# Kernel optimization log

Measured on AMD Instinct MI355X. Metric: run time of the kernel, lower is better.

The kernel has to match this reference:

```python
import jax, jax.numpy as jnp
import numpy as np
from jax import lax

B, N, CIN, COUT, FPS, K, TCH, M, H = 8, 4096, 128, 256, 1024, 24, 256, 32, 4
HD = TCH // H
BN_SCALE = 1.0 / np.sqrt(1.0 + 1e-5)  # eval-mode BN: running_mean=0, running_var=1


def _gather(points, idx):
    # points [B,N,C], idx [B,S] or [B,S,K] -> gathered points
    return jax.vmap(lambda p, i: p[i])(points, idx)


def _bn(x, g, b):
    return x * (g * BN_SCALE) + b


def _ln(x, g, b):
    mu = jnp.mean(x, -1, keepdims=True)
    v = jnp.var(x, -1, keepdims=True)
    return (x - mu) / jnp.sqrt(v + 1e-5) * g + b


def _gelu(x):
    return jax.nn.gelu(x, approximate=False)


def _fps(xyz, npoint, farthest0):
    Bb, Nn, _ = xyz.shape
    def step(carry, _):
        dmin, far = carry
        c = jax.vmap(lambda p, i: p[i])(xyz, far)  # [B,3]
        d = jnp.sum((xyz - c[:, None, :]) ** 2, -1)
        dmin = jnp.minimum(dmin, d)
        return (dmin, jnp.argmax(dmin, -1)), far
    init = (jnp.full((Bb, Nn), 1e10, xyz.dtype), farthest0)
    _, cents = lax.scan(step, init, None, length=npoint)
    return cents.T  # [B, npoint]


def _sqdist(src, dst):
    d = -2.0 * jnp.einsum('bnc,bmc->bnm', src, dst)
    d = d + jnp.sum(src ** 2, -1)[:, :, None]
    d = d + jnp.sum(dst ** 2, -1)[:, None, :]
    return d


def _forward(xyz, x, t, farthest0, Wproj, gproj, bproj, Wl1, gl1, bl1, Wl2, gl2, bl2,
             Wc1, gc1, bc1, Wc2, gc2, bc2, Wq, Wk, Wv, Wo,
             ln1g, ln1b, Wqkv, Wao, ln2g, ln2b, Wf1, Wf2):
    # --- GenerateGraph: FPS + KNN grouping ---
    fps_idx = _fps(xyz, FPS, farthest0)            # [B,S]
    new_xyz = _gather(xyz, fps_idx)                # [B,S,3]
    xT = jnp.transpose(x, (0, 2, 1))               # [B,N,Cin]
    new_pts = _gather(xT, fps_idx)                 # [B,S,Cin]
    dist = _sqdist(new_xyz, xyz)                   # [B,S,N]
    _, idx = lax.top_k(-dist, K)                   # [B,S,K] nearest neighbors
    grouped = _gather(xT, idx)                     # [B,S,K,Cin]
    edge = grouped - new_pts[:, :, None, :]
    # --- Local: Conv1DBR proj + Conv1DBRRes (channels-last, 1x1 convs = GEMM) ---
    h = _gelu(_bn(jnp.einsum('bskc,oc->bsko', edge, Wproj), gproj, bproj))
    r = _gelu(_bn(jnp.einsum('bsko,po->bskp', h, Wl1), gl1, bl1))
    r = _bn(jnp.einsum('bskp,op->bsko', r, Wl2), gl2, bl2)
    h = _gelu(r + h)
    f = jnp.max(h, axis=2)                         # adaptive_max_pool over k -> [B,S,O]
    # --- Channel (ca): Conv1DBRRes on centroid features ---
    r = _gelu(_bn(f @ Wc1.T, gc1, bc1))
    r = _bn(r @ Wc2.T, gc2, bc2)
    f = _gelu(r + f)
    x_out = jnp.transpose(f, (0, 2, 1))            # [B,O,S]
    # --- Local2Former: tokens attend to local features ---
    q = t @ Wq.T
    kk = f @ Wk.T
    v = f @ Wv.T
    a = jax.nn.softmax(jnp.einsum('bmd,bsd->bms', q, kk) * (TCH ** -0.5), axis=-1)
    t = t + jnp.einsum('bms,bsd->bmd', a, v) @ Wo.T
    # --- Former: one pre-norm encoder layer (MHA + MLP) ---
    hn = _ln(t, ln1g, ln1b)
    qkv = (hn @ Wqkv.T).reshape(B, M, 3, H, HD).transpose(2, 0, 3, 1, 4)
    qh, kh, vh = qkv[0], qkv[1], qkv[2]            # [B,H,M,hd]
    attn = jax.nn.softmax(jnp.einsum('bhmd,bhnd->bhmn', qh, kh) * (HD ** -0.5), axis=-1)
    o = jnp.einsum('bhmn,bhnd->bhmd', attn, vh).transpose(0, 2, 1, 3).reshape(B, M, TCH)
    t = t + o @ Wao.T
    hn = _ln(t, ln2g, ln2b)
    t = t + _gelu(hn @ Wf1.T) @ Wf2.T
    return new_xyz, x_out, t


def setup_inputs() -> dict:
    key = jax.random.key(0)
    ks = jax.random.split(key, 40)
    def w(k, o, i):
        return jax.random.normal(k, (o, i), jnp.float32) / np.sqrt(i)
    def g(k, c):
        return 1.0 + 0.1 * jax.random.normal(k, (c,), jnp.float32)
    def bta(k, c):
        return 0.1 * jax.random.normal(k, (c,), jnp.float32)
    inp = {
        'xyz': jax.random.normal(ks[0], (B, N, 3), jnp.float32),
        'x': jax.random.normal(ks[1], (B, CIN, N), jnp.float32),
        't': jax.random.normal(ks[2], (B, M, TCH), jnp.float32),
        'farthest0': jax.random.randint(ks[3], (B,), 0, N),
        'Wproj': w(ks[4], COUT, CIN), 'gproj': g(ks[5], COUT), 'bproj': bta(ks[6], COUT),
        'Wl1': w(ks[7], COUT, COUT), 'gl1': g(ks[8], COUT), 'bl1': bta(ks[9], COUT),
        'Wl2': w(ks[10], COUT, COUT), 'gl2': g(ks[11], COUT), 'bl2': bta(ks[12], COUT),
        'Wc1': w(ks[13], COUT, COUT), 'gc1': g(ks[14], COUT), 'bc1': bta(ks[15], COUT),
        'Wc2': w(ks[16], COUT, COUT), 'gc2': g(ks[17], COUT), 'bc2': bta(ks[18], COUT),
        'Wq': w(ks[19], TCH, TCH), 'Wk': w(ks[20], TCH, COUT), 'Wv': w(ks[21], TCH, COUT),
        'Wo': w(ks[22], TCH, TCH),
        'ln1g': g(ks[23], TCH), 'ln1b': bta(ks[24], TCH),
        'Wqkv': w(ks[25], 3 * TCH, TCH), 'Wao': w(ks[26], TCH, TCH),
        'ln2g': g(ks[27], TCH), 'ln2b': bta(ks[28], TCH),
        'Wf1': w(ks[29], 2 * TCH, TCH), 'Wf2': w(ks[30], TCH, 2 * TCH),
    }
    return inp


def reference(xyz, x, t, farthest0, Wproj, gproj, bproj, Wl1, gl1, bl1, Wl2, gl2, bl2,
              Wc1, gc1, bc1, Wc2, gc2, bc2, Wq, Wk, Wv, Wo,
              ln1g, ln1b, Wqkv, Wao, ln2g, ln2b, Wf1, Wf2):
    return _forward(xyz, x, t, farthest0, Wproj, gproj, bproj, Wl1, gl1, bl1, Wl2, gl2, bl2,
                    Wc1, gc1, bc1, Wc2, gc2, bc2, Wq, Wk, Wv, Wo,
                    ln1g, ln1b, Wqkv, Wao, ln2g, ln2b, Wf1, Wf2)
```

## Files before the change

### kernel.cpp

```cpp
#include <hip/hip_runtime.h>
#include <math.h>

#define Bc 8
#define Nc 4096
#define CINc 128
#define COUTc 256
#define Sc 1024
#define Kc 24
#define TCHc 256
#define Mc 32
#define Hc 4
#define HDc 64
#define MBAT (Sc*Kc)

#define BN_SCALE_F 0.9999950000374997f

typedef __attribute__((ext_vector_type(8))) short bf16x8;
typedef __attribute__((ext_vector_type(4))) float f32x4;

__device__ __forceinline__ float b2f(short s){
  unsigned int u = ((unsigned int)(unsigned short)s) << 16;
  union { unsigned int u; float f; } c; c.u = u; return c.f;
}
__device__ __forceinline__ short f2b(float f){
  union { unsigned int u; float f; } c; c.f = f;
  unsigned int u = c.u;
  unsigned int r = (u + 0x7fffu + ((u >> 16) & 1u)) >> 16;
  return (short)(r & 0xffffu);
}
__device__ __forceinline__ float gelu_f(float v){
  return 0.5f * v * (1.f + erff(v * 0.7071067811865475f));
}
__device__ __forceinline__ float rdval(const float* p){ return *p; }
__device__ __forceinline__ float rdval(const short* p){ return b2f(*p); }
__device__ __forceinline__ void wrval(float* p, float v){ *p = v; }
__device__ __forceinline__ void wrval(short* p, float v){ *p = f2b(v); }

__device__ __forceinline__ void gl_lds16(const short* g, short* l){
  __builtin_amdgcn_global_load_lds(
     (const __attribute__((address_space(1))) void*)g,
     (__attribute__((address_space(3))) void*)l, 16, 0, 0);
}

__device__ __forceinline__ void bar_lds(){
  asm volatile("s_waitcnt lgkmcnt(0)" ::: "memory");
  __builtin_amdgcn_s_barrier();
}

template<int CTRL>
__device__ __forceinline__ double dpp_max_f64(double v){
  long long x = __double_as_longlong(v);
  int lo = (int)(unsigned int)(x & 0xFFFFFFFFLL);
  int hi = (int)(unsigned int)((unsigned long long)x >> 32);
  int plo = __builtin_amdgcn_update_dpp(lo, lo, CTRL, 0xF, 0xF, false);
  int phi = __builtin_amdgcn_update_dpp(hi, hi, CTRL, 0xF, 0xF, false);
  double p = __longlong_as_double((long long)(((unsigned long long)(unsigned int)phi << 32)
                                              | (unsigned int)plo));
  return fmax(v, p);
}
template<int CTRL>
__device__ __forceinline__ float dpp_min_f32(float v){
  int x = __float_as_int(v);
  int p = __builtin_amdgcn_update_dpp(x, x, CTRL, 0xF, 0xF, false);
  return fminf(v, __int_as_float(p));
}
template<int CTRL>
__device__ __forceinline__ float dpp_max_f32(float v){
  int x = __float_as_int(v);
  int p = __builtin_amdgcn_update_dpp(x, x, CTRL, 0xF, 0xF, false);
  return fmaxf(v, __int_as_float(p));
}
template<int CTRL>
__device__ __forceinline__ unsigned dpp_min_u32(unsigned v){
  int p = __builtin_amdgcn_update_dpp((int)v, (int)v, CTRL, 0xF, 0xF, false);
  unsigned pu = (unsigned)p;
  return v < pu ? v : pu;
}
__device__ __forceinline__ float wave_min63(float v){
  v = dpp_min_f32<0x111>(v); v = dpp_min_f32<0x112>(v); v = dpp_min_f32<0x114>(v);
  v = dpp_min_f32<0x118>(v); v = dpp_min_f32<0x142>(v); v = dpp_min_f32<0x143>(v);
  return v;
}
__device__ __forceinline__ float wave_max63(float v){
  v = dpp_max_f32<0x111>(v); v = dpp_max_f32<0x112>(v); v = dpp_max_f32<0x114>(v);
  v = dpp_max_f32<0x118>(v); v = dpp_max_f32<0x142>(v); v = dpp_max_f32<0x143>(v);
  return v;
}
__device__ __forceinline__ float bcast63(float v){
  return __int_as_float(__builtin_amdgcn_readlane(__float_as_int(v), 63));
}

#define PREP_FPS 8
#define PREP_TOTAL 256
#define NWORK 248

__global__ __launch_bounds__(512) void prep_kernel(
    const float* __restrict__ xyz, const int* __restrict__ far0, int* __restrict__ fps_idx,
    const float* __restrict__ x, short* __restrict__ xT,
    const float* __restrict__ Wproj, const float* __restrict__ Wl1, const float* __restrict__ Wl2,
    const float* __restrict__ Wc1, const float* __restrict__ Wc2,
    const float* __restrict__ Wk, const float* __restrict__ Wv,
    const float* __restrict__ Wq, const float* __restrict__ Wo,
    const float* __restrict__ Wqkv, const float* __restrict__ Wao,
    const float* __restrict__ Wf1, const float* __restrict__ Wf2,
    const float* __restrict__ t_in,
    short* __restrict__ wbf,
    int* __restrict__ knn_idx, float* __restrict__ out0){
  __shared__ __align__(16) char smemc[57728];
  int bid = blockIdx.x, tid = threadIdx.x;
  if(bid < PREP_FPS){
    int b = bid;
    float* sxyz = (float*)smemc;
    unsigned short* sid = (unsigned short*)(smemc + 49152);
    int* hist = (int*)(smemc + 57344);
    double* pwave = (double*)(smemc + 57600);
    const float* xb = xyz + (size_t)b*Nc*3;
    if(tid < 64) hist[tid] = 0;
    float gx[8], gy[8], gz[8]; int code[8];
    __syncthreads();
#pragma unroll
    for(int j=0;j<8;j++){
      int n = tid + 512*j;
      const float* p = xb + n*3;
      gx[j]=p[0]; gy[j]=p[1]; gz[j]=p[2];
      int qx = (int)fminf(fmaxf((gx[j]+4.2f)*(4.f/8.4f),0.f),3.f);
      int qy = (int)fminf(fmaxf((gy[j]+4.2f)*(4.f/8.4f),0.f),3.f);
      int qz = (int)fminf(fmaxf((gz[j]+4.2f)*(4.f/8.4f),0.f),3.f);
      code[j] = ((qx>>1)<<5)|((qy>>1)<<4)|((qz>>1)<<3)|((qx&1)<<2)|((qy&1)<<1)|(qz&1);
      atomicAdd(&hist[code[j]], 1);
    }
    __syncthreads();
    if(tid==0){
      int run=0;
      for(int i=0;i<64;i++){ int h=hist[i]; hist[i]=run; run+=h; }
    }
    __syncthreads();
#pragma unroll
    for(int j=0;j<8;j++){
      int slot = atomicAdd(&hist[code[j]], 1);
      sxyz[slot*3]=gx[j]; sxyz[slot*3+1]=gy[j]; sxyz[slot*3+2]=gz[j];
      sid[slot] = (unsigned short)(tid + 512*j);
    }
    __syncthreads();
    float px[8], py[8], pz[8], dmin[8];
    unsigned int lokey[8];
    float mnx=3e38f,mny=3e38f,mnz=3e38f,mxx=-3e38f,mxy=-3e38f,mxz=-3e38f;
#pragma unroll
    for(int j=0;j<8;j++){
      int i = (tid>>6)*512 + j*64 + (tid&63);
      float xx=sxyz[i*3], yy=sxyz[i*3+1], zz=sxyz[i*3+2];
      px[j]=xx; py[j]=yy; pz[j]=zz;
      dmin[j]=1e10f;
      lokey[j]=(unsigned int)((Nc-1) - (int)sid[i]);
      mnx=fminf(mnx,xx); mxx=fmaxf(mxx,xx);
      mny=fminf(mny,yy); mxy=fmaxf(mxy,yy);
      mnz=fminf(mnz,zz); mxz=fmaxf(mxz,zz);
    }
    float bbmnx = bcast63(wave_min63(mnx)), bbmxx = bcast63(wave_max63(mxx));
    float bbmny = bcast63(wave_min63(mny)), bbmxy = bcast63(wave_max63(mxy));
    float bbmnz = bcast63(wave_min63(mnz)), bbmxz = bcast63(wave_max63(mxz));
    __syncthreads();
    for(int i=tid; i<Nc; i+=512){
      const float* p = xb + i*3;
      sxyz[i*3]=p[0]; sxyz[i*3+1]=p[1]; sxyz[i*3+2]=p[2];
    }
    __syncthreads();
    int winner = far0[b] & (Nc-1);
    int* out = fps_idx + b*Sc;
    double pk = 0.0;
    float wm = 3.0e38f;
    for(int it=0; it<Sc; it++){
      if(tid==0)
        __hip_atomic_store(&out[it], winner, __ATOMIC_RELAXED, __HIP_MEMORY_SCOPE_AGENT);
      float cx=sxyz[winner*3], cy=sxyz[winner*3+1], cz=sxyz[winner*3+2];
      float ddx = fmaxf(fmaxf(bbmnx - cx, cx - bbmxx), 0.f);
      float ddy = fmaxf(fmaxf(bbmny - cy, cy - bbmxy), 0.f);
      float ddz = fmaxf(fmaxf(bbmnz - cz, cz - bbmxz), 0.f);
      float md2 = ddx*ddx + ddy*ddy + ddz*ddz;
      if(md2 < wm*1.0001f){
        double key[8];
#pragma unroll
        for(int j=0;j<8;j++){
          float dx = __fsub_rn(px[j], cx);
          float dy = __fsub_rn(py[j], cy);
          float dz = __fsub_rn(pz[j], cz);
          float d = __fadd_rn(__fadd_rn(__fmul_rn(dx,dx), __fmul_rn(dy,dy)), __fmul_rn(dz,dz));
          dmin[j] = fminf(dmin[j], d);
          unsigned long long k = (((unsigned long long)__float_as_uint(dmin[j])) << 32) | lokey[j];
          key[j] = __longlong_as_double((long long)k);
        }
#pragma unroll
        for(int st=4; st>0; st>>=1)
#pragma unroll
          for(int j=0;j<st;j++) key[j] = fmax(key[j], key[j+st]);
        double kv = key[0];
        kv = dpp_max_f64<0x111>(kv);
        kv = dpp_max_f64<0x112>(kv);
        kv = dpp_max_f64<0x114>(kv);
        kv = dpp_max_f64<0x118>(kv);
        kv = dpp_max_f64<0x142>(kv);
        kv = dpp_max_f64<0x143>(kv);
        pk = kv;
        wm = __int_as_float(__builtin_amdgcn_readlane(
               (int)(__double_as_longlong(kv) >> 32), 63));
      }
      int p = it & 1;
      if((tid & 63) == 63) pwave[p*8 + (tid>>6)] = pk;
      bar_lds();
      double k0 = pwave[p*8+0], k1 = pwave[p*8+1], k2 = pwave[p*8+2], k3 = pwave[p*8+3];
      double k4 = pwave[p*8+4], k5 = pwave[p*8+5], k6 = pwave[p*8+6], k7 = pwave[p*8+7];
      double kb = fmax(fmax(fmax(k0,k1), fmax(k2,k3)), fmax(fmax(k4,k5), fmax(k6,k7)));
      unsigned long long kbits = (unsigned long long)__double_as_longlong(kb);
      winner = (Nc-1) - (int)(kbits & 0xFFFFFFFFULL);
    }
  } else {
    int wid = bid - PREP_FPS;
    int b = wid / 31;
    int widb = wid % 31;
    short (*tile)[33] = (short(*)[33])smemc;
    for(int t = wid; t < 4096; t += NWORK){
      int bb = t >> 9;
      int rem = t & 511;
      int n0 = (rem & 127) * 32;
      int c0 = (rem >> 7) * 32;
      int tx = tid & 31, ty = tid >> 5;
      __syncthreads();
#pragma unroll
      for(int i=0;i<32;i+=16)
        tile[ty+i][tx] = f2b(x[((size_t)bb*CINc + (c0+ty+i))*Nc + n0+tx]);
      __syncthreads();
#pragma unroll
      for(int i=0;i<32;i+=16)
        xT[((size_t)bb*Nc + (n0+ty+i))*CINc + c0+tx] = tile[tx][ty+i];
    }
    {
      int gid = wid*512 + tid;
      const int stride = NWORK*512;
      short* p = wbf;
      for(int i=gid; i<COUTc*CINc; i+=stride) p[i] = f2b(Wproj[i]);
      p += COUTc*CINc;
      for(int i=gid; i<COUTc*COUTc; i+=stride) p[i] = f2b(Wl1[i]);
      p += COUTc*COUTc;
      for(int i=gid; i<COUTc*COUTc; i+=stride) p[i] = f2b(Wl2[i]);
      p += COUTc*COUTc;
      for(int i=gid; i<COUTc*COUTc; i+=stride) p[i] = f2b(Wc1[i]);
      p += COUTc*COUTc;
      for(int i=gid; i<COUTc*COUTc; i+=stride) p[i] = f2b(Wc2[i]);
      p += COUTc*COUTc;
      for(int i=gid; i<TCHc*COUTc; i+=stride) p[i] = f2b(Wk[i]);
      p += TCHc*COUTc;
      for(int i=gid; i<TCHc*COUTc; i+=stride) p[i] = f2b(Wv[i]);
      p += TCHc*COUTc;
      for(int i=gid; i<TCHc*TCHc; i+=stride) p[i] = f2b(Wq[i]);
      p += TCHc*TCHc;
      for(int i=gid; i<TCHc*TCHc; i+=stride) p[i] = f2b(Wo[i]);
      p += TCHc*TCHc;
      for(int i=gid; i<3*TCHc*TCHc; i+=stride) p[i] = f2b(Wqkv[i]);
      p += 3*TCHc*TCHc;
      for(int i=gid; i<TCHc*TCHc; i+=stride) p[i] = f2b(Wao[i]);
      p += TCHc*TCHc;
      for(int i=gid; i<2*TCHc*TCHc; i+=stride) p[i] = f2b(Wf1[i]);
      p += 2*TCHc*TCHc;
      for(int i=gid; i<2*TCHc*TCHc; i+=stride) p[i] = f2b(Wf2[i]);
      p += 2*TCHc*TCHc;
      for(int i=gid; i<Bc*Mc*TCHc; i+=stride) p[i] = f2b(t_in[i]);
    }
    int* s_qn = (int*)smemc;
    float* pv = (float*)(smemc + 32);
    int*   pi = (int*)(smemc + 64);
    const float* xb = xyz + (size_t)b*Nc*3;
    float px[8], py[8], pz[8], db[8];
#pragma unroll
    for(int j=0;j<8;j++){
      int n = tid + 512*j;
      float xx=xb[n*3], yy=xb[n*3+1], zz=xb[n*3+2];
      px[j]=xx; py[j]=yy; pz[j]=zz;
      db[j] = __fadd_rn(__fadd_rn(__fmul_rn(xx,xx),__fmul_rn(yy,yy)),__fmul_rn(zz,zz));
    }
    __syncthreads();
    for(int s = widb; s < Sc; s += 31){
      if(tid==0){
        int qn;
        for(;;){
          qn = __hip_atomic_load(&fps_idx[b*Sc + s], __ATOMIC_RELAXED, __HIP_MEMORY_SCOPE_AGENT);
          if(qn >= 0) break;
          __builtin_amdgcn_s_sleep(8);
        }
        s_qn[0] = qn & (Nc-1);
      }
      bar_lds();
      int qn = s_qn[0];
      const float* q = xyz + ((size_t)b*Nc + qn)*3;
      float sxq = q[0], syq = q[1], szq = q[2];
      if(tid < 3) out0[((size_t)b*Sc + s)*3 + tid] = q[tid];
      float ss = __fadd_rn(__fadd_rn(__fmul_rn(sxq,sxq),__fmul_rn(syq,syq)),__fmul_rn(szq,szq));
      float dv[8];
#pragma unroll
      for(int j=0;j<8;j++){
        float e = __fmul_rn(sxq,px[j]);
        e = __fadd_rn(e, __fmul_rn(syq,py[j]));
        e = __fadd_rn(e, __fmul_rn(szq,pz[j]));
        dv[j] = __fadd_rn(__fadd_rn(__fmul_rn(-2.f,e), ss), db[j]);
      }
      int* ob = knn_idx + ((size_t)b*Sc + s)*Kc;
      for(int k=0;k<Kc;k++){
        float bvv = dv[0];
#pragma unroll
        for(int j=1;j<8;j++) bvv = fminf(bvv, dv[j]);
        bvv = dpp_min_f32<0x111>(bvv);
        bvv = dpp_min_f32<0x112>(bvv);
        bvv = dpp_min_f32<0x114>(bvv);
        bvv = dpp_min_f32<0x118>(bvv);
        bvv = dpp_min_f32<0x142>(bvv);
        bvv = dpp_min_f32<0x143>(bvv);
        if((tid&63)==63) pv[tid>>6] = bvv;
        bar_lds();
        float vmin = fminf(fminf(fminf(pv[0],pv[1]), fminf(pv[2],pv[3])),
                           fminf(fminf(pv[4],pv[5]), fminf(pv[6],pv[7])));
        unsigned bi = 0xFFFFFFFFu;
#pragma unroll
        for(int j=0;j<8;j++){
          unsigned n = (unsigned)(tid + 512*j);
          if(dv[j]==vmin && n < bi) bi = n;
        }
        bi = dpp_min_u32<0x111>(bi);
        bi = dpp_min_u32<0x112>(bi);
        bi = dpp_min_u32<0x114>(bi);
        bi = dpp_min_u32<0x118>(bi);
        bi = dpp_min_u32<0x142>(bi);
        bi = dpp_min_u32<0x143>(bi);
        if((tid&63)==63) pi[tid>>6] = (int)bi;
        bar_lds();
        unsigned win = (unsigned)pi[0];
#pragma unroll
        for(int w=1;w<8;w++){ unsigned u=(unsigned)pi[w]; win = u<win?u:win; }
        if(tid==0) ob[k] = (int)(win & (Nc-1));
#pragma unroll
        for(int j=0;j<8;j++) if((int)win == tid + 512*j) dv[j] = 3.4e38f;
      }
    }
  }
}

template<int HAS_BN, int HAS_GELU, int HAS_RES, typename TRES>
__global__ __launch_bounds__(256) void gemm128(
    const short* __restrict__ A, const short* __restrict__ W,
    const float* __restrict__ g, const float* __restrict__ bias,
    const TRES* __restrict__ Res, short* __restrict__ Out,
    int Nn, int Kk){
  __shared__ short As[128*32];
  __shared__ short Bs[128*32];
  int bm = blockIdx.y*128, bn = blockIdx.x*128;
  int tid = threadIdx.x;
  int wave = tid>>6, lane = tid&63, quad = lane>>4, l16 = lane&15;
  int wr = (wave>>1)*64, wc = (wave&1)*64;
  f32x4 acc[4][4];
#pragma unroll
  for(int i=0;i<4;i++)
#pragma unroll
    for(int j=0;j<4;j++) acc[i][j] = (f32x4){0.f,0.f,0.f,0.f};
  int sr = tid>>2, scc = (tid&3)*8;
  const short* Ap = A + (size_t)(bm+sr)*Kk + scc;
  const short* Wp = W + (size_t)(bn+sr)*Kk + scc;
  for(int k0=0; k0<Kk; k0+=32){
    gl_lds16(Ap + k0,                    As + tid*8);
    gl_lds16(Ap + k0 + (size_t)64*Kk,    As + 2048 + tid*8);
    gl_lds16(Wp + k0,                    Bs + tid*8);
    gl_lds16(Wp + k0 + (size_t)64*Kk,    Bs + 2048 + tid*8);
    __syncthreads();
    bf16x8 af[4], bfr[4];
#pragma unroll
    for(int mt=0; mt<4; mt++) af[mt]  = *(const bf16x8*)&As[(wr+mt*16+l16)*32 + quad*8];
#pragma unroll
    for(int nt=0; nt<4; nt++) bfr[nt] = *(const bf16x8*)&Bs[(wc+nt*16+l16)*32 + quad*8];
#pragma unroll
    for(int mt=0; mt<4; mt++)
#pragma unroll
      for(int nt=0; nt<4; nt++)
        acc[mt][nt] = __builtin_amdgcn_mfma_f32_16x16x32_bf16(af[mt], bfr[nt], acc[mt][nt], 0, 0, 0);
    __syncthreads();
  }
#pragma unroll
  for(int nt=0; nt<4; nt++){
    int col = bn + wc + nt*16 + l16;
    float gs = 0.f, bs_ = 0.f;
    if(HAS_BN){ gs = g[col] * BN_SCALE_F; bs_ = bias[col]; }
#pragma unroll
    for(int mt=0; mt<4; mt++){
#pragma unroll
      for(int r2=0;r2<4;r2++){
        int row = bm + wr + mt*16 + quad*4 + r2;
        float v = acc[mt][nt][r2];
        if(HAS_BN) v = v*gs + bs_;
        if(HAS_RES) v += rdval(Res + (size_t)row*Nn + col);
        if(HAS_GELU) v = gelu_f(v);
        Out[(size_t)row*Nn + col] = f2b(v);
      }
    }
  }
}

__global__ __launch_bounds__(256) void proj128(
    const short* __restrict__ xT, const int* __restrict__ knn_idx, const int* __restrict__ fps_idx,
    const short* __restrict__ W, const float* __restrict__ g, const float* __restrict__ bias,
    short* __restrict__ Out, int R0){
  __shared__ short As[128*32];
  __shared__ short Bs[128*32];
  int bm = blockIdx.y*128, bn = blockIdx.x*128;
  int tid = threadIdx.x;
  int wave = tid>>6, lane = tid&63, quad = lane>>4, l16 = lane&15;
  int wr = (wave>>1)*64, wc = (wave&1)*64;
  f32x4 acc[4][4];
#pragma unroll
  for(int i=0;i<4;i++)
#pragma unroll
    for(int j=0;j<4;j++) acc[i][j] = (f32x4){0.f,0.f,0.f,0.f};
  int sr = tid>>2, scc = (tid&3)*8;
  int Rg0 = R0 + bm + sr, Rg1 = Rg0 + 64;
  int b0 = Rg0 / (Sc*Kc), b1 = Rg1 / (Sc*Kc);
  int nk0 = knn_idx[Rg0] & (Nc-1), nk1 = knn_idx[Rg1] & (Nc-1);
  int nc0 = fps_idx[Rg0 / Kc] & (Nc-1), nc1 = fps_idx[Rg1 / Kc] & (Nc-1);
  const short* pk0 = xT + ((size_t)b0*Nc + nk0)*CINc + scc;
  const short* pc0 = xT + ((size_t)b0*Nc + nc0)*CINc + scc;
  const short* pk1 = xT + ((size_t)b1*Nc + nk1)*CINc + scc;
  const short* pc1 = xT + ((size_t)b1*Nc + nc1)*CINc + scc;
  const short* Wp  = W + (size_t)(bn+sr)*CINc + scc;
  for(int k0=0; k0<CINc; k0+=32){
    gl_lds16(Wp + k0,                      Bs + tid*8);
    gl_lds16(Wp + k0 + (size_t)64*CINc,    Bs + 2048 + tid*8);
    bf16x8 vk = *(const bf16x8*)(pk0 + k0);
    bf16x8 vc = *(const bf16x8*)(pc0 + k0);
    bf16x8 e0, e1;
#pragma unroll
    for(int i=0;i<8;i++) e0[i] = f2b(__fsub_rn(b2f(vk[i]), b2f(vc[i])));
    vk = *(const bf16x8*)(pk1 + k0);
    vc = *(const bf16x8*)(pc1 + k0);
#pragma unroll
    for(int i=0;i<8;i++) e1[i] = f2b(__fsub_rn(b2f(vk[i]), b2f(vc[i])));
    *(bf16x8*)&As[tid*8] = e0;
    *(bf16x8*)&As[2048 + tid*8] = e1;
    __syncthreads();
    bf16x8 af[4], bfr[4];
#pragma unroll
    for(int mt=0; mt<4; mt++) af[mt]  = *(const bf16x8*)&As[(wr+mt*16+l16)*32 + quad*8];
#pragma unroll
    for(int nt=0; nt<4; nt++) bfr[nt] = *(const bf16x8*)&Bs[(wc+nt*16+l16)*32 + quad*8];
#pragma unroll
    for(int mt=0; mt<4; mt++)
#pragma unroll
      for(int nt=0; nt<4; nt++)
        acc[mt][nt] = __builtin_amdgcn_mfma_f32_16x16x32_bf16(af[mt], bfr[nt], acc[mt][nt], 0, 0, 0);
    __syncthreads();
  }
#pragma unroll
  for(int nt=0; nt<4; nt++){
    int col = bn + wc + nt*16 + l16;
    float gs = g[col] * BN_SCALE_F, bs_ = bias[col];
#pragma unroll
    for(int mt=0; mt<4; mt++){
#pragma unroll
      for(int r2=0;r2<4;r2++){
        int row = bm + wr + mt*16 + quad*4 + r2;
        float v = acc[mt][nt][r2]*gs + bs_;
        Out[(size_t)row*COUTc + col] = f2b(gelu_f(v));
      }
    }
  }
}

__global__ __launch_bounds__(192) void gemm_l2max(
    const short* __restrict__ A, const short* __restrict__ W,
    const float* __restrict__ g, const float* __restrict__ bias,
    const short* __restrict__ Hres, short* __restrict__ Fout, int R0){
  __shared__ short As[48*32];
  __shared__ short Bs[64*32];
  __shared__ float sm[48][65];
  int bm = blockIdx.y*48, bn = blockIdx.x*64;
  int tid = threadIdx.x;
  int wave = tid >> 6, lane = tid & 63, quad = lane >> 4, l16 = lane & 15;
  f32x4 acc[4];
#pragma unroll
  for(int i=0;i<4;i++) acc[i] = (f32x4){0.f,0.f,0.f,0.f};
  const short* Ap  = A + (size_t)(bm + (tid>>2))*COUTc + (tid&3)*8;
  const short* Wp  = W + (size_t)(bn + (tid>>2))*COUTc + (tid&3)*8;
  const short* Wp2 = W + (size_t)(bn + 48 + (lane>>2))*COUTc + (lane&3)*8;
  for(int k0=0; k0<COUTc; k0+=32){
    gl_lds16(Ap + k0, As + tid*8);
    gl_lds16(Wp + k0, Bs + tid*8);
    if(wave==0) gl_lds16(Wp2 + k0, Bs + 1536 + lane*8);
    __syncthreads();
    bf16x8 a = *(const bf16x8*)&As[(wave*16 + l16)*32 + quad*8];
#pragma unroll
    for(int ct=0; ct<4; ct++){
      bf16x8 bb = *(const bf16x8*)&Bs[(ct*16 + l16)*32 + quad*8];
      acc[ct] = __builtin_amdgcn_mfma_f32_16x16x32_bf16(a, bb, acc[ct], 0, 0, 0);
    }
    __syncthreads();
  }
#pragma unroll
  for(int ct=0; ct<4; ct++){
    int col = bn + ct*16 + l16;
    float gs = g[col] * BN_SCALE_F, bs_ = bias[col];
#pragma unroll
    for(int r2=0;r2<4;r2++){
      int rl = wave*16 + quad*4 + r2;
      float v = acc[ct][r2]*gs + bs_;
      v += b2f(Hres[(size_t)(bm+rl)*COUTc + col]);
      sm[rl][ct*16 + l16] = gelu_f(v);
    }
  }
  __syncthreads();
  if(tid < 128){
    int gl = tid >> 6, col = tid & 63;
    float mx = -3.4e38f;
#pragma unroll
    for(int kk=0; kk<Kc; kk++) mx = fmaxf(mx, sm[gl*Kc + kk][col]);
    int gg = R0/Kc + blockIdx.y*2 + gl;
    Fout[(size_t)gg*COUTc + bn + col] = f2b(mx);
  }
}

template<int HAS_BN, int HAS_GELU, int HAS_RES, typename TRES, typename TOUT>
__global__ __launch_bounds__(256) void gemm64d(
    const short* __restrict__ A, const short* __restrict__ W,
    const float* __restrict__ g, const float* __restrict__ bias,
    const TRES* __restrict__ Res, TOUT* __restrict__ Out,
    int Nn, int Kk){
  __shared__ short As[64*32];
  __shared__ short Bs[64*32];
  int bm = blockIdx.y*64, bn = blockIdx.x*64;
  int tid = threadIdx.x;
  int wave = tid >> 6, lane = tid & 63, quad = lane >> 4, l16 = lane & 15;
  f32x4 acc[4];
#pragma unroll
  for(int i=0;i<4;i++) acc[i] = (f32x4){0.f,0.f,0.f,0.f};
  const short* Ap = A + (size_t)(bm + (tid>>2))*Kk + (tid&3)*8;
  const short* Wp = W + (size_t)(bn + (tid>>2))*Kk + (tid&3)*8;
  for(int k0=0; k0<Kk; k0+=32){
    gl_lds16(Ap + k0, As + tid*8);
    gl_lds16(Wp + k0, Bs + tid*8);
    __syncthreads();
    bf16x8 a = *(const bf16x8*)&As[(wave*16 + l16)*32 + quad*8];
#pragma unroll
    for(int ct=0; ct<4; ct++){
      bf16x8 bb = *(const bf16x8*)&Bs[(ct*16 + l16)*32 + quad*8];
      acc[ct] = __builtin_amdgcn_mfma_f32_16x16x32_bf16(a, bb, acc[ct], 0, 0, 0);
    }
    __syncthreads();
  }
#pragma unroll
  for(int ct=0; ct<4; ct++){
    int col = bn + ct*16 + l16;
    float gs = 0.f, bs_ = 0.f;
    if(HAS_BN){ gs = g[col] * BN_SCALE_F; bs_ = bias[col]; }
#pragma unroll
    for(int r2=0;r2<4;r2++){
      int row = bm + wave*16 + quad*4 + r2;
      float v = acc[ct][r2];
      if(HAS_BN) v = v*gs + bs_;
      if(HAS_RES) v += rdval(Res + (size_t)row*Nn + col);
      if(HAS_GELU) v = gelu_f(v);
      wrval(Out + (size_t)row*Nn + col, v);
    }
  }
}

__global__ __launch_bounds__(256) void transpose_f(const short* __restrict__ f2, float* __restrict__ out1){
  __shared__ short tile[32][33];
  int b = blockIdx.z;
  int s0 = blockIdx.x*32, c0 = blockIdx.y*32;
  int tx = threadIdx.x & 31, ty = threadIdx.x >> 5;
#pragma unroll
  for(int i=0;i<32;i+=8)
    tile[ty+i][tx] = f2[((size_t)b*Sc + (s0+ty+i))*COUTc + c0+tx];
  __syncthreads();
#pragma unroll
  for(int i=0;i<32;i+=8)
    out1[((size_t)b*COUTc + (c0+ty+i))*Sc + s0+tx] = b2f(tile[tx][ty+i]);
}

__global__ __launch_bounds__(256) void l2f_attn(
    const short* __restrict__ qb, const short* __restrict__ kv,
    short* __restrict__ ao){
  int blk = blockIdx.x; int b = blk / Mc; int m = blk % Mc;
  int tid = threadIdx.x;
  __shared__ float qs[TCHc];
  __shared__ float aw[Sc];
  __shared__ float red[8];
  qs[tid] = b2f(qb[(size_t)(b*Mc+m)*TCHc + tid]);
  __syncthreads();
  float sc[4];
#pragma unroll
  for(int jj=0;jj<4;jj++){
    int j = tid + 256*jj;
    const short* kp = kv + ((size_t)b*Sc + j)*512;
    float a = 0.f;
    for(int c=0;c<TCHc;c+=8){
      bf16x8 v8 = *(const bf16x8*)(kp + c);
#pragma unroll
      for(int i=0;i<8;i++) a += b2f(v8[i]) * qs[c+i];
    }
    sc[jj] = a * 0.0625f;
  }
  float mx = fmaxf(fmaxf(sc[0],sc[1]), fmaxf(sc[2],sc[3]));
#pragma unroll
  for(int off=32; off>0; off>>=1) mx = fmaxf(mx, __shfl_xor(mx, off));
  if((tid&63)==0) red[tid>>6] = mx;
  __syncthreads();
  mx = fmaxf(fmaxf(red[0],red[1]), fmaxf(red[2],red[3]));
  float se = 0.f;
#pragma unroll
  for(int jj=0;jj<4;jj++){
    float e = expf(sc[jj] - mx);
    aw[tid + 256*jj] = e;
    se += e;
  }
#pragma unroll
  for(int off=32; off>0; off>>=1) se += __shfl_xor(se, off);
  if((tid&63)==0) red[4 + (tid>>6)] = se;
  __syncthreads();
  se = red[4]+red[5]+red[6]+red[7];
  float inv = 1.f/se;
#pragma unroll
  for(int jj=0;jj<4;jj++) aw[tid + 256*jj] *= inv;
  __syncthreads();
  float acc = 0.f;
  const short* vp = kv + (size_t)b*Sc*512 + 256 + tid;
  for(int j=0;j<Sc;j++) acc += aw[j] * b2f(vp[(size_t)j*512]);
  ao[(size_t)(b*Mc+m)*TCHc + tid] = f2b(acc);
}

__global__ __launch_bounds__(64) void former_attn(const short* __restrict__ qkv, short* __restrict__ oa){
  int blk = blockIdx.x;
  int m = blk % Mc; int bh = blk / Mc; int h = bh % Hc; int b = bh / Hc;
  int lane = threadIdx.x;
  __shared__ float qs[HDc];
  __shared__ float aw2[32];
  const short* base = qkv + (size_t)(b*Mc)*(3*TCHc);
  qs[lane] = b2f(base[(size_t)m*3*TCHc + h*HDc + lane]);
  __syncthreads();
  int j = lane & 31;
  const short* kp = base + (size_t)j*3*TCHc + TCHc + h*HDc;
  float s = 0.f;
  for(int d=0; d<HDc; d+=8){
    bf16x8 v8 = *(const bf16x8*)(kp + d);
#pragma unroll
    for(int i=0;i<8;i++) s += b2f(v8[i]) * qs[d+i];
  }
  s *= 0.125f;
  float mx = s;
#pragma unroll
  for(int off=16; off>0; off>>=1) mx = fmaxf(mx, __shfl_xor(mx, off, 32));
  float e = expf(s - mx);
  float se = e;
#pragma unroll
  for(int off=16; off>0; off>>=1) se += __shfl_xor(se, off, 32);
  if(lane < 32) aw2[lane] = e / se;
  __syncthreads();
  float acc = 0.f;
  const short* vp = base + 2*TCHc + h*HDc + lane;
  for(int jj=0; jj<32; jj++) acc += aw2[jj] * b2f(vp[(size_t)jj*3*TCHc]);
  oa[(size_t)(b*Mc+m)*TCHc + h*HDc + lane] = f2b(acc);
}

__global__ __launch_bounds__(64) void ln_kernel(const float* __restrict__ X, const float* __restrict__ g,
                                                const float* __restrict__ bb, short* __restrict__ O){
  int row = blockIdx.x, lane = threadIdx.x;
  const float* xp = X + (size_t)row*TCHc;
  float x[4];
#pragma unroll
  for(int j2=0;j2<4;j2++) x[j2] = xp[lane + 64*j2];
  float sm = x[0]+x[1]+x[2]+x[3];
#pragma unroll
  for(int off=32; off>0; off>>=1) sm += __shfl_xor(sm, off);
  float mu = sm * (1.f/256.f);
  float vs = 0.f;
#pragma unroll
  for(int j2=0;j2<4;j2++){ float d = x[j2]-mu; vs += d*d; }
#pragma unroll
  for(int off=32; off>0; off>>=1) vs += __shfl_xor(vs, off);
  float var = vs * (1.f/256.f);
  float rstd = 1.f / sqrtf(var + 1e-5f);
#pragma unroll
  for(int j2=0;j2<4;j2++){
    int c = lane + 64*j2;
    float o = (x[j2]-mu)*rstd*g[c] + bb[c];
    O[(size_t)row*TCHc + c] = f2b(o);
  }
}

extern "C" void kernel_launch(void* const* d_in, const int* in_sizes, int n_in,
                              void* d_out, int out_size, void* d_ws, size_t ws_size,
                              hipStream_t stream){
  const float* xyz  = (const float*)d_in[0];
  const float* x    = (const float*)d_in[1];
  const float* t_in = (const float*)d_in[2];
  const int*   far0 = (const int*)d_in[3];
  const float* Wproj=(const float*)d_in[4];  const float* gproj=(const float*)d_in[5];  const float* bproj=(const float*)d_in[6];
  const float* Wl1 = (const float*)d_in[7];  const float* gl1 = (const float*)d_in[8];  const float* bl1 = (const float*)d_in[9];
  const float* Wl2 = (const float*)d_in[10]; const float* gl2 = (const float*)d_in[11]; const float* bl2 = (const float*)d_in[12];
  const float* Wc1 = (const float*)d_in[13]; const float* gc1 = (const float*)d_in[14]; const float* bc1 = (const float*)d_in[15];
  const float* Wc2 = (const float*)d_in[16]; const float* gc2 = (const float*)d_in[17]; const float* bc2 = (const float*)d_in[18];
  const float* Wq  = (const float*)d_in[19]; const float* Wk  = (const float*)d_in[20]; const float* Wv  = (const float*)d_in[21];
  const float* Wo  = (const float*)d_in[22];
  const float* ln1g= (const float*)d_in[23]; const float* ln1b= (const float*)d_in[24];
  const float* Wqkv= (const float*)d_in[25]; const float* Wao = (const float*)d_in[26];
  const float* ln2g= (const float*)d_in[27]; const float* ln2b= (const float*)d_in[28];
  const float* Wf1 = (const float*)d_in[29]; const float* Wf2 = (const float*)d_in[30];

  char* wsb = (char*)d_ws;
  size_t off = 0;
  auto alloc = [&](size_t bytes)->void*{ void* p = wsb + off; off += (bytes + 255) & ~(size_t)255; return p; };
  int*   fps_i = (int*)alloc((size_t)Bc*Sc*4);
  int*   knn   = (int*)alloc((size_t)Bc*Sc*Kc*4);
  short* xT    = (short*)alloc((size_t)Bc*Nc*CINc*2);
  size_t wbf_elems = (size_t)COUTc*CINc + 4*(size_t)COUTc*COUTc + 2*(size_t)TCHc*COUTc
                   + 2*(size_t)TCHc*TCHc + 3*(size_t)TCHc*TCHc + (size_t)TCHc*TCHc
                   + 2*(size_t)TCHc*TCHc + 2*(size_t)TCHc*TCHc + (size_t)Bc*Mc*TCHc;
  short* wbf   = (short*)alloc(wbf_elems*2);
  short* fbuf  = (short*)alloc((size_t)Bc*Sc*COUTc*2);
  short* rcbuf = (short*)alloc((size_t)Bc*Sc*COUTc*2);
  short* f2buf = (short*)alloc((size_t)Bc*Sc*COUTc*2);
  short* kvbuf = (short*)alloc((size_t)Bc*Sc*512*2);
  short* qbuf  = (short*)alloc((size_t)Bc*Mc*TCHc*2);
  short* a1out = (short*)alloc((size_t)Bc*Mc*TCHc*2);
  float* t1buf = (float*)alloc((size_t)Bc*Mc*TCHc*4);
  short* hnbuf = (short*)alloc((size_t)Bc*Mc*TCHc*2);
  short* qkvb  = (short*)alloc((size_t)Bc*Mc*3*TCHc*2);
  short* a2out = (short*)alloc((size_t)Bc*Mc*TCHc*2);
  float* t2buf = (float*)alloc((size_t)Bc*Mc*TCHc*4);
  short* hn2buf= (short*)alloc((size_t)Bc*Mc*TCHc*2);
  short* g1buf = (short*)alloc((size_t)Bc*Mc*2*TCHc*2);
  size_t full_bytes  = (size_t)Bc*MBAT*COUTc*2;
  size_t batch_bytes = (size_t)MBAT*COUTc*2;
  bool batched = (off + 2*(full_bytes + 256) <= ws_size);
  short* hbuf = (short*)alloc(batched ? full_bytes : batch_bytes);
  short* rbuf = (short*)alloc(batched ? full_bytes : batch_bytes);
  if(off > ws_size) return;

  short* wproj_bf = wbf;
  short* wl1_bf   = wproj_bf + COUTc*CINc;
  short* wl2_bf   = wl1_bf + COUTc*COUTc;
  short* wc1_bf   = wl2_bf + COUTc*COUTc;
  short* wc2_bf   = wc1_bf + COUTc*COUTc;
  short* wkv_bf   = wc2_bf + COUTc*COUTc;
  short* wq_bf    = wkv_bf + 2*TCHc*COUTc;
  short* wo_bf    = wq_bf + TCHc*TCHc;
  short* wqkv_bf  = wo_bf + TCHc*TCHc;
  short* wao_bf   = wqkv_bf + 3*TCHc*TCHc;
  short* wf1_bf   = wao_bf + TCHc*TCHc;
  short* wf2_bf   = wf1_bf + 2*TCHc*TCHc;
  short* tbf      = wf2_bf + 2*TCHc*TCHc;

  float* out0 = (float*)d_out;
  float* out1 = out0 + (size_t)Bc*Sc*3;
  float* out2 = out1 + (size_t)Bc*COUTc*Sc;

  hipMemsetAsync(fps_i, 0xFF, (size_t)Bc*Sc*4, stream);
  prep_kernel<<<PREP_TOTAL, 512, 0, stream>>>(xyz, far0, fps_i, x, xT,
                                              Wproj, Wl1, Wl2, Wc1, Wc2, Wk, Wv,
                                              Wq, Wo, Wqkv, Wao, Wf1, Wf2, t_in,
                                              wbf, knn, out0);
  if(batched){
    proj128<<<dim3(COUTc/128, (Bc*MBAT)/128), 256, 0, stream>>>(xT, knn, fps_i, wproj_bf, gproj, bproj, hbuf, 0);
    gemm128<1,1,0,short><<<dim3(COUTc/128, (Bc*MBAT)/128), 256, 0, stream>>>(hbuf, wl1_bf, gl1, bl1, (const short*)nullptr, rbuf, COUTc, COUTc);
    gemm_l2max<<<dim3(COUTc/64, (Bc*MBAT)/48), 192, 0, stream>>>(rbuf, wl2_bf, gl2, bl2, hbuf, fbuf, 0);
  } else {
    for(int b=0; b<Bc; b++){
      proj128<<<dim3(COUTc/128, MBAT/128), 256, 0, stream>>>(xT, knn, fps_i, wproj_bf, gproj, bproj, hbuf, b*MBAT);
      gemm128<1,1,0,short><<<dim3(COUTc/128, MBAT/128), 256, 0, stream>>>(hbuf, wl1_bf, gl1, bl1, (const short*)nullptr, rbuf, COUTc, COUTc);
      gemm_l2max<<<dim3(COUTc/64, MBAT/48), 192, 0, stream>>>(rbuf, wl2_bf, gl2, bl2, hbuf, fbuf, b*MBAT);
    }
  }
  gemm64d<1,1,0,short,short><<<dim3(COUTc/64, (Bc*Sc)/64), 256, 0, stream>>>(fbuf, wc1_bf, gc1, bc1, (const short*)nullptr, rcbuf, COUTc, COUTc);
  gemm64d<1,1,1,short,short><<<dim3(COUTc/64, (Bc*Sc)/64), 256, 0, stream>>>(rcbuf, wc2_bf, gc2, bc2, fbuf, f2buf, COUTc, COUTc);
  transpose_f<<<dim3(Sc/32, COUTc/32, Bc), 256, 0, stream>>>(f2buf, out1);
  gemm64d<0,0,0,short,short><<<dim3(TCHc/64, (Bc*Mc)/64), 256, 0, stream>>>(tbf, wq_bf, nullptr, nullptr, (const short*)nullptr, qbuf, TCHc, TCHc);
  gemm64d<0,0,0,short,short><<<dim3(512/64, (Bc*Sc)/64), 256, 0, stream>>>(f2buf, wkv_bf, nullptr, nullptr, (const short*)nullptr, kvbuf, 512, COUTc);
  l2f_attn<<<Bc*Mc, 256, 0, stream>>>(qbuf, kvbuf, a1out);
  gemm64d<0,0,1,float,float><<<dim3(TCHc/64, (Bc*Mc)/64), 256, 0, stream>>>(a1out, wo_bf, nullptr, nullptr, t_in, t1buf, TCHc, TCHc);
  ln_kernel<<<Bc*Mc, 64, 0, stream>>>(t1buf, ln1g, ln1b, hnbuf);
  gemm64d<0,0,0,short,short><<<dim3((3*TCHc)/64, (Bc*Mc)/64), 256, 0, stream>>>(hnbuf, wqkv_bf, nullptr, nullptr, (const short*)nullptr, qkvb, 3*TCHc, TCHc);
  former_attn<<<Bc*Hc*Mc, 64, 0, stream>>>(qkvb, a2out);
  gemm64d<0,0,1,float,float><<<dim3(TCHc/64, (Bc*Mc)/64), 256, 0, stream>>>(a2out, wao_bf, nullptr, nullptr, t1buf, t2buf, TCHc, TCHc);
  ln_kernel<<<Bc*Mc, 64, 0, stream>>>(t2buf, ln2g, ln2b, hn2buf);
  gemm64d<0,1,0,short,short><<<dim3((2*TCHc)/64, (Bc*Mc)/64), 256, 0, stream>>>(hn2buf, wf1_bf, nullptr, nullptr, (const short*)nullptr, g1buf, 2*TCHc, TCHc);
  gemm64d<0,0,1,float,float><<<dim3(TCHc/64, (Bc*Mc)/64), 256, 0, stream>>>(g1buf, wf2_bf, nullptr, nullptr, t2buf, out2, TCHc, 2*TCHc);
}
```

Measured before the change: 1.132 ms.

## Fuse local proj, residual conv pair and neighbor max-pool into one kernel

Replaces the three separate local-stage kernels (gather+proj GEMM, L1 GEMM, L2 GEMM+residual+max) with one kernel per pair of groups (48 rows). Each block keeps its edge features, projected features and intermediate activations in LDS, so the large [B*S*K, 256] intermediate buffers never go through global memory. The cost is that every block reloads all three weight matrices from global/L2, with small 48-row tiles and about 76KB of LDS per block, which limits occupancy and gives lower MFMA reuse per weight load.

```diff
diff --git a/kernel.cpp b/kernel.cpp
--- a/kernel.cpp
+++ b/kernel.cpp
@@ -342,181 +342,161 @@
   }
 }
 
-template<int HAS_BN, int HAS_GELU, int HAS_RES, typename TRES>
-__global__ __launch_bounds__(256) void gemm128(
-    const short* __restrict__ A, const short* __restrict__ W,
-    const float* __restrict__ g, const float* __restrict__ bias,
-    const TRES* __restrict__ Res, short* __restrict__ Out,
-    int Nn, int Kk){
-  __shared__ short As[128*32];
-  __shared__ short Bs[128*32];
-  int bm = blockIdx.y*128, bn = blockIdx.x*128;
+__global__ __launch_bounds__(256) void local_fused(
+    const short* __restrict__ xT, const int* __restrict__ knn_idx, const int* __restrict__ fps_idx,
+    const short* __restrict__ Wp_, const float* __restrict__ gp, const float* __restrict__ bp,
+    const short* __restrict__ W1, const float* __restrict__ g1, const float* __restrict__ b1,
+    const short* __restrict__ W2, const float* __restrict__ g2, const float* __restrict__ b2,
+    short* __restrict__ Fout){
+  __shared__ __align__(16) char lds[77824];
+  short* Asrc = (short*)lds;
+  short* Wst  = (short*)(lds + 12288);
+  short* Hb   = (short*)(lds + 28672);
+  short* Rb   = (short*)(lds + 53248);
+  int p = blockIdx.x;
+  int R0 = p*48;
   int tid = threadIdx.x;
-  int wave = tid>>6, lane = tid&63, quad = lane>>4, l16 = lane&15;
-  int wr = (wave>>1)*64, wc = (wave&1)*64;
-  f32x4 acc[4][4];
-#pragma unroll
-  for(int i=0;i<4;i++)
-#pragma unroll
-    for(int j=0;j<4;j++) acc[i][j] = (f32x4){0.f,0.f,0.f,0.f};
-  int sr = tid>>2, scc = (tid&3)*8;
-  const short* Ap = A + (size_t)(bm+sr)*Kk + scc;
-  const short* Wp = W + (size_t)(bn+sr)*Kk + scc;
-  for(int k0=0; k0<Kk; k0+=32){
-    gl_lds16(Ap + k0,                    As + tid*8);
-    gl_lds16(Ap + k0 + (size_t)64*Kk,    As + 2048 + tid*8);
-    gl_lds16(Wp + k0,                    Bs + tid*8);
-    gl_lds16(Wp + k0 + (size_t)64*Kk,    Bs + 2048 + tid*8);
-    __syncthreads();
-    bf16x8 af[4], bfr[4];
-#pragma unroll
-    for(int mt=0; mt<4; mt++) af[mt]  = *(const bf16x8*)&As[(wr+mt*16+l16)*32 + quad*8];
-#pragma unroll
-    for(int nt=0; nt<4; nt++) bfr[nt] = *(const bf16x8*)&Bs[(wc+nt*16+l16)*32 + quad*8];
-#pragma unroll
-    for(int mt=0; mt<4; mt++)
-#pragma unroll
-      for(int nt=0; nt<4; nt++)
+  int w = tid >> 6, lane = tid & 63, quad = lane >> 4, l16 = lane & 15;
+  int colbase = w*64;
+#pragma unroll
+  for(int u0=0; u0<3; u0++){
+    int u = tid + u0*256;
+    int r = u >> 4, seg = u & 15;
+    int Rg = R0 + r;
+    int bb = Rg / MBAT;
+    int nk = knn_idx[Rg] & (Nc-1);
+    int nc = fps_idx[Rg / Kc] & (Nc-1);
+    bf16x8 vk = *(const bf16x8*)(xT + ((size_t)bb*Nc + nk)*CINc + seg*8);
+    bf16x8 vc = *(const bf16x8*)(xT + ((size_t)bb*Nc + nc)*CINc + seg*8);
+    bf16x8 e;
+#pragma unroll
+    for(int i=0;i<8;i++) e[i] = f2b(__fsub_rn(b2f(vk[i]), b2f(vc[i])));
+    *(bf16x8*)&Asrc[((seg>>2)*48 + r)*32 + (seg&3)*8] = e;
+  }
+  __syncthreads();
+  f32x4 acc[3][4];
+#pragma unroll
+  for(int mt=0;mt<3;mt++)
+#pragma unroll
+    for(int nt=0;nt<4;nt++) acc[mt][nt] = (f32x4){0.f,0.f,0.f,0.f};
+  for(int k0=0; k0<CINc; k0+=32){
+#pragma unroll
+    for(int c=0;c<4;c++)
+      gl_lds16(Wp_ + (size_t)(c*64 + (tid>>2))*CINc + k0 + (tid&3)*8,
+               Wst + c*2048 + tid*8);
+    __syncthreads();
+    bf16x8 af[3], bfr[4];
+#pragma unroll
+    for(int mt=0;mt<3;mt++) af[mt] = *(const bf16x8*)&Asrc[(((k0>>5))*48 + mt*16 + l16)*32 + quad*8];
+#pragma unroll
+    for(int nt=0;nt<4;nt++) bfr[nt] = *(const bf16x8*)&Wst[(colbase + nt*16 + l16)*32 + quad*8];
+#pragma unroll
+    for(int mt=0;mt<3;mt++)
+#pragma unroll
+      for(int nt=0;nt<4;nt++)
         acc[mt][nt] = __builtin_amdgcn_mfma_f32_16x16x32_bf16(af[mt], bfr[nt], acc[mt][nt], 0, 0, 0);
     __syncthreads();
   }
 #pragma unroll
-  for(int nt=0; nt<4; nt++){
-    int col = bn + wc + nt*16 + l16;
-    float gs = 0.f, bs_ = 0.f;
-    if(HAS_BN){ gs = g[col] * BN_SCALE_F; bs_ = bias[col]; }
-#pragma unroll
-    for(int mt=0; mt<4; mt++){
+  for(int nt=0;nt<4;nt++){
+    int col = colbase + nt*16 + l16;
+    float gs = gp[col] * BN_SCALE_F, bs_ = bp[col];
+    int kb = col >> 5, kr = col & 31;
+#pragma unroll
+    for(int mt=0;mt<3;mt++)
 #pragma unroll
       for(int r2=0;r2<4;r2++){
-        int row = bm + wr + mt*16 + quad*4 + r2;
-        float v = acc[mt][nt][r2];
-        if(HAS_BN) v = v*gs + bs_;
-        if(HAS_RES) v += rdval(Res + (size_t)row*Nn + col);
-        if(HAS_GELU) v = gelu_f(v);
-        Out[(size_t)row*Nn + col] = f2b(v);
+        int row = mt*16 + quad*4 + r2;
+        float v = acc[mt][nt][r2]*gs + bs_;
+        Hb[(kb*48 + row)*32 + kr] = f2b(gelu_f(v));
       }
-    }
-  }
-}
-
-__global__ __launch_bounds__(256) void proj128(
-    const short* __restrict__ xT, const int* __restrict__ knn_idx, const int* __restrict__ fps_idx,
-    const short* __restrict__ W, const float* __restrict__ g, const float* __restrict__ bias,
-    short* __restrict__ Out, int R0){
-  __shared__ short As[128*32];
-  __shared__ short Bs[128*32];
-  int bm = blockIdx.y*128, bn = blockIdx.x*128;
-  int tid = threadIdx.x;
-  int wave = tid>>6, lane = tid&63, quad = lane>>4, l16 = lane&15;
-  int wr = (wave>>1)*64, wc = (wave&1)*64;
-  f32x4 acc[4][4];
-#pragma unroll
-  for(int i=0;i<4;i++)
-#pragma unroll
-    for(int j=0;j<4;j++) acc[i][j] = (f32x4){0.f,0.f,0.f,0.f};
-  int sr = tid>>2, scc = (tid&3)*8;
-  int Rg0 = R0 + bm + sr, Rg1 = Rg0 + 64;
-  int b0 = Rg0 / (Sc*Kc), b1 = Rg1 / (Sc*Kc);
-  int nk0 = knn_idx[Rg0] & (Nc-1), nk1 = knn_idx[Rg1] & (Nc-1);
-  int nc0 = fps_idx[Rg0 / Kc] & (Nc-1), nc1 = fps_idx[Rg1 / Kc] & (Nc-1);
-  const short* pk0 = xT + ((size_t)b0*Nc + nk0)*CINc + scc;
-  const short* pc0 = xT + ((size_t)b0*Nc + nc0)*CINc + scc;
-  const short* pk1 = xT + ((size_t)b1*Nc + nk1)*CINc + scc;
-  const short* pc1 = xT + ((size_t)b1*Nc + nc1)*CINc + scc;
-  const short* Wp  = W + (size_t)(bn+sr)*CINc + scc;
-  for(int k0=0; k0<CINc; k0+=32){
-    gl_lds16(Wp + k0,                      Bs + tid*8);
-    gl_lds16(Wp + k0 + (size_t)64*CINc,    Bs + 2048 + tid*8);
-    bf16x8 vk = *(const bf16x8*)(pk0 + k0);
-    bf16x8 vc = *(const bf16x8*)(pc0 + k0);
-    bf16x8 e0, e1;
-#pragma unroll
-    for(int i=0;i<8;i++) e0[i] = f2b(__fsub_rn(b2f(vk[i]), b2f(vc[i])));
-    vk = *(const bf16x8*)(pk1 + k0);
-    vc = *(const bf16x8*)(pc1 + k0);
-#pragma unroll
-    for(int i=0;i<8;i++) e1[i] = f2b(__fsub_rn(b2f(vk[i]), b2f(vc[i])));
-    *(bf16x8*)&As[tid*8] = e0;
-    *(bf16x8*)&As[2048 + tid*8] = e1;
-    __syncthreads();
-    bf16x8 af[4], bfr[4];
-#pragma unroll
-    for(int mt=0; mt<4; mt++) af[mt]  = *(const bf16x8*)&As[(wr+mt*16+l16)*32 + quad*8];
-#pragma unroll
-    for(int nt=0; nt<4; nt++) bfr[nt] = *(const bf16x8*)&Bs[(wc+nt*16+l16)*32 + quad*8];
-#pragma unroll
-    for(int mt=0; mt<4; mt++)
-#pragma unroll
-      for(int nt=0; nt<4; nt++)
+  }
+  __syncthreads();
+#pragma unroll
+  for(int mt=0;mt<3;mt++)
+#pragma unroll
+    for(int nt=0;nt<4;nt++) acc[mt][nt] = (f32x4){0.f,0.f,0.f,0.f};
+  for(int k0=0; k0<COUTc; k0+=32){
+#pragma unroll
+    for(int c=0;c<4;c++)
+      gl_lds16(W1 + (size_t)(c*64 + (tid>>2))*COUTc + k0 + (tid&3)*8,
+               Wst + c*2048 + tid*8);
+    __syncthreads();
+    bf16x8 af[3], bfr[4];
+#pragma unroll
+    for(int mt=0;mt<3;mt++) af[mt] = *(const bf16x8*)&Hb[(((k0>>5))*48 + mt*16 + l16)*32 + quad*8];
+#pragma unroll
+    for(int nt=0;nt<4;nt++) bfr[nt] = *(const bf16x8*)&Wst[(colbase + nt*16 + l16)*32 + quad*8];
+#pragma unroll
+    for(int mt=0;mt<3;mt++)
+#pragma unroll
+      for(int nt=0;nt<4;nt++)
         acc[mt][nt] = __builtin_amdgcn_mfma_f32_16x16x32_bf16(af[mt], bfr[nt], acc[mt][nt], 0, 0, 0);
     __syncthreads();
   }
 #pragma unroll
-  for(int nt=0; nt<4; nt++){
-    int col = bn + wc + nt*16 + l16;
-    float gs = g[col] * BN_SCALE_F, bs_ = bias[col];
-#pragma unroll
-    for(int mt=0; mt<4; mt++){
+  for(int nt=0;nt<4;nt++){
+    int col = colbase + nt*16 + l16;
+    float gs = g1[col] * BN_SCALE_F, bs_ = b1[col];
+    int kb = col >> 5, kr = col & 31;
+#pragma unroll
+    for(int mt=0;mt<3;mt++)
 #pragma unroll
       for(int r2=0;r2<4;r2++){
-        int row = bm + wr + mt*16 + quad*4 + r2;
+        int row = mt*16 + quad*4 + r2;
         float v = acc[mt][nt][r2]*gs + bs_;
-        Out[(size_t)row*COUTc + col] = f2b(gelu_f(v));
+        Rb[(kb*48 + row)*32 + kr] = f2b(gelu_f(v));
       }
-    }
-  }
-}
-
-__global__ __launch_bounds__(192) void gemm_l2max(
-    const short* __restrict__ A, const short* __restrict__ W,
-    const float* __restrict__ g, const float* __restrict__ bias,
-    const short* __restrict__ Hres, short* __restrict__ Fout, int R0){
-  __shared__ short As[48*32];
-  __shared__ short Bs[64*32];
-  __shared__ float sm[48][65];
-  int bm = blockIdx.y*48, bn = blockIdx.x*64;
-  int tid = threadIdx.x;
-  int wave = tid >> 6, lane = tid & 63, quad = lane >> 4, l16 = lane & 15;
-  f32x4 acc[4];
-#pragma unroll
-  for(int i=0;i<4;i++) acc[i] = (f32x4){0.f,0.f,0.f,0.f};
-  const short* Ap  = A + (size_t)(bm + (tid>>2))*COUTc + (tid&3)*8;
-  const short* Wp  = W + (size_t)(bn + (tid>>2))*COUTc + (tid&3)*8;
-  const short* Wp2 = W + (size_t)(bn + 48 + (lane>>2))*COUTc + (lane&3)*8;
+  }
+  __syncthreads();
+#pragma unroll
+  for(int mt=0;mt<3;mt++)
+#pragma unroll
+    for(int nt=0;nt<4;nt++) acc[mt][nt] = (f32x4){0.f,0.f,0.f,0.f};
   for(int k0=0; k0<COUTc; k0+=32){
-    gl_lds16(Ap + k0, As + tid*8);
-    gl_lds16(Wp + k0, Bs + tid*8);
-    if(wave==0) gl_lds16(Wp2 + k0, Bs + 1536 + lane*8);
-    __syncthreads();
-    bf16x8 a = *(const bf16x8*)&As[(wave*16 + l16)*32 + quad*8];
-#pragma unroll
-    for(int ct=0; ct<4; ct++){
-      bf16x8 bb = *(const bf16x8*)&Bs[(ct*16 + l16)*32 + quad*8];
-      acc[ct] = __builtin_amdgcn_mfma_f32_16x16x32_bf16(a, bb, acc[ct], 0, 0, 0);
-    }
-    __syncthreads();
-  }
-#pragma unroll
-  for(int ct=0; ct<4; ct++){
-    int col = bn + ct*16 + l16;
-    float gs = g[col] * BN_SCALE_F, bs_ = bias[col];
-#pragma unroll
-    for(int r2=0;r2<4;r2++){
-      int rl = wave*16 + quad*4 + r2;
-      float v = acc[ct][r2]*gs + bs_;
-      v += b2f(Hres[(size_t)(bm+rl)*COUTc + col]);
-      sm[rl][ct*16 + l16] = gelu_f(v);
-    }
-  }
-  __syncthreads();
-  if(tid < 128){
-    int gl = tid >> 6, col = tid & 63;
-    float mx = -3.4e38f;
-#pragma unroll
-    for(int kk=0; kk<Kc; kk++) mx = fmaxf(mx, sm[gl*Kc + kk][col]);
-    int gg = R0/Kc + blockIdx.y*2 + gl;
-    Fout[(size_t)gg*COUTc + bn + col] = f2b(mx);
+#pragma unroll
+    for(int c=0;c<4;c++)
+      gl_lds16(W2 + (size_t)(c*64 + (tid>>2))*COUTc + k0 + (tid&3)*8,
+               Wst + c*2048 + tid*8);
+    __syncthreads();
+    bf16x8 af[3], bfr[4];
+#pragma unroll
+    for(int mt=0;mt<3;mt++) af[mt] = *(const bf16x8*)&Rb[(((k0>>5))*48 + mt*16 + l16)*32 + quad*8];
+#pragma unroll
+    for(int nt=0;nt<4;nt++) bfr[nt] = *(const bf16x8*)&Wst[(colbase + nt*16 + l16)*32 + quad*8];
+#pragma unroll
+    for(int mt=0;mt<3;mt++)
+#pragma unroll
+      for(int nt=0;nt<4;nt++)
+        acc[mt][nt] = __builtin_amdgcn_mfma_f32_16x16x32_bf16(af[mt], bfr[nt], acc[mt][nt], 0, 0, 0);
+    __syncthreads();
+  }
+#pragma unroll
+  for(int nt=0;nt<4;nt++){
+    int col = colbase + nt*16 + l16;
+    float gs = g2[col] * BN_SCALE_F, bs_ = b2[col];
+    int kb = col >> 5, kr = col & 31;
+    float gm0 = -3.4e38f, gm1 = -3.4e38f;
+#pragma unroll
+    for(int mt=0;mt<3;mt++)
+#pragma unroll
+      for(int r2=0;r2<4;r2++){
+        int row = mt*16 + quad*4 + r2;
+        float v = acc[mt][nt][r2]*gs + bs_;
+        v += b2f(Hb[(kb*48 + row)*32 + kr]);
+        v = gelu_f(v);
+        if(mt==0) gm0 = fmaxf(gm0, v);
+        else if(mt==2) gm1 = fmaxf(gm1, v);
+        else { if(quad < 2) gm0 = fmaxf(gm0, v); else gm1 = fmaxf(gm1, v); }
+      }
+    gm0 = fmaxf(gm0, __shfl_xor(gm0, 16));
+    gm0 = fmaxf(gm0, __shfl_xor(gm0, 32));
+    gm1 = fmaxf(gm1, __shfl_xor(gm1, 16));
+    gm1 = fmaxf(gm1, __shfl_xor(gm1, 32));
+    if(quad == 0){
+      Fout[(size_t)(p*2)*COUTc + col]     = f2b(gm0);
+      Fout[(size_t)(p*2+1)*COUTc + col]   = f2b(gm1);
+    }
   }
 }
 
@@ -731,11 +711,6 @@
   float* t2buf = (float*)alloc((size_t)Bc*Mc*TCHc*4);
   short* hn2buf= (short*)alloc((size_t)Bc*Mc*TCHc*2);
   short* g1buf = (short*)alloc((size_t)Bc*Mc*2*TCHc*2);
-  size_t full_bytes  = (size_t)Bc*MBAT*COUTc*2;
-  size_t batch_bytes = (size_t)MBAT*COUTc*2;
-  bool batched = (off + 2*(full_bytes + 256) <= ws_size);
-  short* hbuf = (short*)alloc(batched ? full_bytes : batch_bytes);
-  short* rbuf = (short*)alloc(batched ? full_bytes : batch_bytes);
   if(off > ws_size) return;
 
   short* wproj_bf = wbf;
@@ -761,17 +736,10 @@
                                               Wproj, Wl1, Wl2, Wc1, Wc2, Wk, Wv,
                                               Wq, Wo, Wqkv, Wao, Wf1, Wf2, t_in,
                                               wbf, knn, out0);
-  if(batched){
-    proj128<<<dim3(COUTc/128, (Bc*MBAT)/128), 256, 0, stream>>>(xT, knn, fps_i, wproj_bf, gproj, bproj, hbuf, 0);
-    gemm128<1,1,0,short><<<dim3(COUTc/128, (Bc*MBAT)/128), 256, 0, stream>>>(hbuf, wl1_bf, gl1, bl1, (const short*)nullptr, rbuf, COUTc, COUTc);
-    gemm_l2max<<<dim3(COUTc/64, (Bc*MBAT)/48), 192, 0, stream>>>(rbuf, wl2_bf, gl2, bl2, hbuf, fbuf, 0);
-  } else {
-    for(int b=0; b<Bc; b++){
-      proj128<<<dim3(COUTc/128, MBAT/128), 256, 0, stream>>>(xT, knn, fps_i, wproj_bf, gproj, bproj, hbuf, b*MBAT);
-      gemm128<1,1,0,short><<<dim3(COUTc/128, MBAT/128), 256, 0, stream>>>(hbuf, wl1_bf, gl1, bl1, (const short*)nullptr, rbuf, COUTc, COUTc);
-      gemm_l2max<<<dim3(COUTc/64, MBAT/48), 192, 0, stream>>>(rbuf, wl2_bf, gl2, bl2, hbuf, fbuf, b*MBAT);
-    }
-  }
+  local_fused<<<(Bc*Sc)/2, 256, 0, stream>>>(xT, knn, fps_i,
+                                             wproj_bf, gproj, bproj,
+                                             wl1_bf, gl1, bl1,
+                                             wl2_bf, gl2, bl2, fbuf);
   gemm64d<1,1,0,short,short><<<dim3(COUTc/64, (Bc*Sc)/64), 256, 0, stream>>>(fbuf, wc1_bf, gc1, bc1, (const short*)nullptr, rcbuf, COUTc, COUTc);
   gemm64d<1,1,1,short,short><<<dim3(COUTc/64, (Bc*Sc)/64), 256, 0, stream>>>(rcbuf, wc2_bf, gc2, bc2, fbuf, f2buf, COUTc, COUTc);
   transpose_f<<<dim3(Sc/32, COUTc/32, Bc), 256, 0, stream>>>(f2buf, out1);
```

After: 1.100 ms. 1.03x faster.
